# Kernel optimization log

Measured on AMD Instinct MI355X. Metric: run time of the kernel, lower is better.

## Reference

```python
import jax, jax.numpy as jnp
import numpy as np

N = 50000      # nodes
E = 800000     # edges (avg degree 16)
D_IN = 128
HID = 128
OUT = 64


def setup_inputs() -> dict:
    key = jax.random.key(0)
    ks = jax.random.split(key, 10)
    s = 0.05
    return {
        "node_feats": jax.random.normal(ks[0], (N, D_IN), jnp.float32),
        "edge_index": jax.random.randint(ks[1], (2, E), 0, N, jnp.int32),
        "W1": jax.random.normal(ks[2], (D_IN, HID), jnp.float32) * s,
        "b1": jnp.zeros((HID,), jnp.float32),
        "W2": jax.random.normal(ks[3], (HID, HID), jnp.float32) * s,
        "b2": jnp.zeros((HID,), jnp.float32),
        "W3": jax.random.normal(ks[4], (HID, OUT), jnp.float32) * s,
        "b3": jnp.zeros((OUT,), jnp.float32),
        "skip_W": jax.random.normal(ks[5], (HID, OUT), jnp.float32) * s,
        "skip_b": jnp.zeros((OUT,), jnp.float32),
    }


def _gcn(h, src, dst, out_norm, in_norm, W, b):
    # DGL GraphConv, norm='both': scale src by out_deg^-1/2, sum over incoming
    # edges at dst, scale by in_deg^-1/2, then linear transform + bias.
    h = h * out_norm[:, None]                                   # [N, d]
    agg = jax.ops.segment_sum(h[src], dst, num_segments=N)      # [N, d]
    return (agg * in_norm[:, None]) @ W + b


def reference(node_feats, edge_index, W1, b1, W2, b2, W3, b3, skip_W, skip_b):
    src, dst = edge_index[0], edge_index[1]
    ones = jnp.ones((E,), jnp.float32)
    out_deg = jax.ops.segment_sum(ones, src, num_segments=N)
    in_deg = jax.ops.segment_sum(ones, dst, num_segments=N)
    out_norm = jnp.maximum(out_deg, 1.0) ** -0.5
    in_norm = jnp.maximum(in_deg, 1.0) ** -0.5

    # layer 0 (no skip) + ReLU
    h = jax.nn.relu(_gcn(node_feats, src, dst, out_norm, in_norm, W1, b1))
    # layer 1: same-dim residual blend + ReLU
    g2 = _gcn(h, src, dst, out_norm, in_norm, W2, b2)
    h = jax.nn.relu(0.6 * h + 0.4 * g2)
    # layer 2 (last, no ReLU): dims differ -> projected skip blend
    g3 = _gcn(h, src, dst, out_norm, in_norm, W3, b3)
    h = 0.6 * (h @ skip_W + skip_b) + 0.4 * g3
    return h[None]  # [1, N, OUT]
```

## Files before the change

kernel.cpp:

```cpp
#include <hip/hip_runtime.h>
#include <math.h>

#define TPB 256
#define CAP 64

__global__ __launch_bounds__(TPB) void k_count(const int* __restrict__ ei, int E,
                                               int* __restrict__ cnt, int* __restrict__ od,
                                               unsigned short* __restrict__ slots) {
    int t = blockIdx.x * TPB + threadIdx.x;
    int base = t * 4;
    if (base + 3 < E) {
        int4 s4 = *(const int4*)(ei + base);
        int4 d4 = *(const int4*)(ei + E + base);
        int p0 = atomicAdd(&cnt[d4.x], 1);
        int p1 = atomicAdd(&cnt[d4.y], 1);
        int p2 = atomicAdd(&cnt[d4.z], 1);
        int p3 = atomicAdd(&cnt[d4.w], 1);
        atomicAdd(&od[s4.x], 1);
        atomicAdd(&od[s4.y], 1);
        atomicAdd(&od[s4.z], 1);
        atomicAdd(&od[s4.w], 1);
        if (p0 < CAP) slots[(d4.x << 6) + p0] = (unsigned short)s4.x;
        if (p1 < CAP) slots[(d4.y << 6) + p1] = (unsigned short)s4.y;
        if (p2 < CAP) slots[(d4.z << 6) + p2] = (unsigned short)s4.z;
        if (p3 < CAP) slots[(d4.w << 6) + p3] = (unsigned short)s4.w;
    } else {
        for (int e = base; e < E; ++e) {
            int s = ei[e], d = ei[E + e];
            int pos = atomicAdd(&cnt[d], 1);
            if (pos < CAP) slots[(d << 6) + pos] = (unsigned short)s;
            atomicAdd(&od[s], 1);
        }
    }
}

__global__ __launch_bounds__(TPB) void k_norm(const int* __restrict__ od, const int* __restrict__ cnt,
                                              float* __restrict__ onr, float* __restrict__ rsq,
                                              float* __restrict__ inr, int N) {
    int i = blockIdx.x * TPB + threadIdx.x;
    if (i < N) {
        float o = fmaxf((float)od[i], 1.0f);
        float q = sqrtf(o);
        onr[i] = 1.0f / q;
        rsq[i] = q;
        inr[i] = 1.0f / sqrtf(fmaxf((float)cnt[i], 1.0f));
    }
}

template <bool WONR>
__global__ __launch_bounds__(TPB) void k_spmm(const float* __restrict__ h,
                                              const int* __restrict__ cnt,
                                              const unsigned short* __restrict__ slots,
                                              const float* __restrict__ onr, const float* __restrict__ inr,
                                              float* __restrict__ agg, int N) {
    int lane = threadIdx.x & 63;
    int r = blockIdx.x * 4 + (threadIdx.x >> 6);
    if (r >= N) return;
    int n = cnt[r]; if (n > CAP) n = CAP;
    const unsigned short* sl = slots + (r << 6);
    const float2* hp = (const float2*)h;
    float ax0 = 0.f, ay0 = 0.f, ax1 = 0.f, ay1 = 0.f;
    float ax2 = 0.f, ay2 = 0.f, ax3 = 0.f, ay3 = 0.f;
    int e = 0;
    for (; e + 7 < n; e += 8) {
        ushort4 qa = *(const ushort4*)(sl + e);
        ushort4 qb = *(const ushort4*)(sl + e + 4);
        float2 v0 = hp[qa.x * 64 + lane];
        float2 v1 = hp[qa.y * 64 + lane];
        float2 v2 = hp[qa.z * 64 + lane];
        float2 v3 = hp[qa.w * 64 + lane];
        float2 v4 = hp[qb.x * 64 + lane];
        float2 v5 = hp[qb.y * 64 + lane];
        float2 v6 = hp[qb.z * 64 + lane];
        float2 v7 = hp[qb.w * 64 + lane];
        if (WONR) {
            float w0 = onr[qa.x], w1 = onr[qa.y], w2 = onr[qa.z], w3 = onr[qa.w];
            float w4 = onr[qb.x], w5 = onr[qb.y], w6 = onr[qb.z], w7 = onr[qb.w];
            ax0 += w0 * v0.x + w1 * v1.x;  ay0 += w0 * v0.y + w1 * v1.y;
            ax1 += w2 * v2.x + w3 * v3.x;  ay1 += w2 * v2.y + w3 * v3.y;
            ax2 += w4 * v4.x + w5 * v5.x;  ay2 += w4 * v4.y + w5 * v5.y;
            ax3 += w6 * v6.x + w7 * v7.x;  ay3 += w6 * v6.y + w7 * v7.y;
        } else {
            ax0 += v0.x + v1.x;  ay0 += v0.y + v1.y;
            ax1 += v2.x + v3.x;  ay1 += v2.y + v3.y;
            ax2 += v4.x + v5.x;  ay2 += v4.y + v5.y;
            ax3 += v6.x + v7.x;  ay3 += v6.y + v7.y;
        }
    }
    for (; e + 3 < n; e += 4) {
        ushort4 qa = *(const ushort4*)(sl + e);
        float2 v0 = hp[qa.x * 64 + lane];
        float2 v1 = hp[qa.y * 64 + lane];
        float2 v2 = hp[qa.z * 64 + lane];
        float2 v3 = hp[qa.w * 64 + lane];
        if (WONR) {
            float w0 = onr[qa.x], w1 = onr[qa.y], w2 = onr[qa.z], w3 = onr[qa.w];
            ax0 += w0 * v0.x + w1 * v1.x;  ay0 += w0 * v0.y + w1 * v1.y;
            ax1 += w2 * v2.x + w3 * v3.x;  ay1 += w2 * v2.y + w3 * v3.y;
        } else {
            ax0 += v0.x + v1.x;  ay0 += v0.y + v1.y;
            ax1 += v2.x + v3.x;  ay1 += v2.y + v3.y;
        }
    }
    for (; e < n; ++e) {
        int s0 = sl[e];
        float2 v0 = hp[s0 * 64 + lane];
        float w0 = WONR ? onr[s0] : 1.0f;
        ax0 += w0 * v0.x;  ay0 += w0 * v0.y;
    }
    float sc = inr[r];
    float2 o;
    o.x = sc * ((ax0 + ax1) + (ax2 + ax3));
    o.y = sc * ((ay0 + ay1) + (ay2 + ay3));
    ((float2*)agg)[r * 64 + lane] = o;
}

__global__ __launch_bounds__(TPB) void k_spmm_final(const float* __restrict__ P,
                                                    const int* __restrict__ cnt,
                                                    const unsigned short* __restrict__ slots,
                                                    const float* __restrict__ inr,
                                                    const float* __restrict__ b3, const float* __restrict__ bs,
                                                    float* __restrict__ out, int N) {
    int lane = threadIdx.x & 63;
    int r = blockIdx.x * 4 + (threadIdx.x >> 6);
    if (r >= N) return;
    int n = cnt[r]; if (n > CAP) n = CAP;
    const unsigned short* sl = slots + (r << 6);
    const float* t = P + 64;
    float a0 = 0.f, a1 = 0.f, a2 = 0.f, a3 = 0.f;
    float a4 = 0.f, a5 = 0.f, a6 = 0.f, a7 = 0.f;
    int e = 0;
    for (; e + 7 < n; e += 8) {
        ushort4 qa = *(const ushort4*)(sl + e);
        ushort4 qb = *(const ushort4*)(sl + e + 4);
        a0 += t[qa.x * 128 + lane];
        a1 += t[qa.y * 128 + lane];
        a2 += t[qa.z * 128 + lane];
        a3 += t[qa.w * 128 + lane];
        a4 += t[qb.x * 128 + lane];
        a5 += t[qb.y * 128 + lane];
        a6 += t[qb.z * 128 + lane];
        a7 += t[qb.w * 128 + lane];
    }
    for (; e + 3 < n; e += 4) {
        ushort4 qa = *(const ushort4*)(sl + e);
        a0 += t[qa.x * 128 + lane];
        a1 += t[qa.y * 128 + lane];
        a2 += t[qa.z * 128 + lane];
        a3 += t[qa.w * 128 + lane];
    }
    for (; e < n; ++e) a0 += t[sl[e] * 128 + lane];
    float g3 = inr[r] * (((a0 + a1) + (a2 + a3)) + ((a4 + a5) + (a6 + a7))) + b3[lane];
    float skip = P[r * 128 + lane] + bs[lane];
    out[r * 64 + lane] = 0.6f * skip + 0.4f * g3;
}

template <int MODE>
__global__ __launch_bounds__(TPB) void k_gemm(const float* __restrict__ A,
                                              const float* __restrict__ Wa, const float* __restrict__ Wb,
                                              const float* __restrict__ bias, const float* __restrict__ H,
                                              const float* __restrict__ onr, const float* __restrict__ rsq,
                                              float* __restrict__ C, int N) {
    __shared__ float As[64][132];
    int t = threadIdx.x;
    int bm = blockIdx.x * 64;
#pragma unroll
    for (int rep = 0; rep < 8; ++rep) {
        int idx = rep * TPB + t;
        int i = idx >> 5;
        int k4 = (idx & 31) * 4;
        int row = bm + i;
        float4 v = make_float4(0.f, 0.f, 0.f, 0.f);
        if (row < N) {
            v = *(const float4*)(&A[row * 128 + k4]);
            if (MODE == 2) {
                float rs = rsq[row];
                v.x *= rs; v.y *= rs; v.z *= rs; v.w *= rs;
            }
        }
        *(float4*)(&As[i][k4]) = v;
    }
    __syncthreads();
    int tx = t & 31, ty = t >> 5;
    int j0 = tx * 4;
    const float* Wp;
    int jj, ldw;
    if (MODE == 2) { Wp = (j0 < 64) ? Wa : Wb; jj = j0 & 63; ldw = 64; }
    else           { Wp = Wa;                   jj = j0;      ldw = 128; }
    float4 acc[8];
#pragma unroll
    for (int q = 0; q < 8; ++q) acc[q] = make_float4(0.f, 0.f, 0.f, 0.f);
    for (int k = 0; k < 128; k += 4) {
        float4 w0 = *(const float4*)(&Wp[(k + 0) * ldw + jj]);
        float4 w1 = *(const float4*)(&Wp[(k + 1) * ldw + jj]);
        float4 w2 = *(const float4*)(&Wp[(k + 2) * ldw + jj]);
        float4 w3 = *(const float4*)(&Wp[(k + 3) * ldw + jj]);
#pragma unroll
        for (int q = 0; q < 8; ++q) {
            float4 a = *(const float4*)(&As[ty + 8 * q][k]);
            acc[q].x += a.x * w0.x + a.y * w1.x + a.z * w2.x + a.w * w3.x;
            acc[q].y += a.x * w0.y + a.y * w1.y + a.z * w2.y + a.w * w3.y;
            acc[q].z += a.x * w0.z + a.y * w1.z + a.z * w2.z + a.w * w3.z;
            acc[q].w += a.x * w0.w + a.y * w1.w + a.z * w2.w + a.w * w3.w;
        }
    }
    float4 bv = make_float4(0.f, 0.f, 0.f, 0.f);
    if (MODE != 2) bv = *(const float4*)(&bias[j0]);
#pragma unroll
    for (int q = 0; q < 8; ++q) {
        int row = bm + ty + 8 * q;
        if (row >= N) continue;
        float4 o;
        o.x = acc[q].x + bv.x;
        o.y = acc[q].y + bv.y;
        o.z = acc[q].z + bv.z;
        o.w = acc[q].w + bv.w;
        if (MODE == 1) {
            float hs = rsq[row];
            float4 h = *(const float4*)(&H[row * 128 + j0]);
            o.x = 0.6f * h.x * hs + 0.4f * o.x;
            o.y = 0.6f * h.y * hs + 0.4f * o.y;
            o.z = 0.6f * h.z * hs + 0.4f * o.z;
            o.w = 0.6f * h.w * hs + 0.4f * o.w;
        }
        if (MODE != 2) {
            float on = onr[row];
            o.x = fmaxf(o.x, 0.f) * on;
            o.y = fmaxf(o.y, 0.f) * on;
            o.z = fmaxf(o.z, 0.f) * on;
            o.w = fmaxf(o.w, 0.f) * on;
        } else if (j0 >= 64) {
            float on = onr[row];
            o.x *= on; o.y *= on; o.z *= on; o.w *= on;
        }
        *(float4*)(&C[row * 128 + j0]) = o;
    }
}

extern "C" void kernel_launch(void* const* d_in, const int* in_sizes, int n_in,
                              void* d_out, int out_size, void* d_ws, size_t ws_size,
                              hipStream_t stream) {
    const float* x  = (const float*)d_in[0];
    const int*   ei = (const int*)d_in[1];
    const float* W1 = (const float*)d_in[2];
    const float* b1 = (const float*)d_in[3];
    const float* W2 = (const float*)d_in[4];
    const float* b2 = (const float*)d_in[5];
    const float* W3 = (const float*)d_in[6];
    const float* b3 = (const float*)d_in[7];
    const float* Ws = (const float*)d_in[8];
    const float* bs = (const float*)d_in[9];
    float* out = (float*)d_out;

    int N = in_sizes[0] / 128;
    int E = in_sizes[1] / 2;

    char* p = (char*)d_ws;
    auto alloc = [&](size_t bytes) -> char* {
        char* r = p;
        p += (bytes + 255) & ~(size_t)255;
        return r;
    };
    size_t npad = ((size_t)N * 4 + 255) & ~(size_t)255;
    int*   cnt  = (int*)alloc(npad);
    int*   od   = (int*)alloc(npad);
    float* onr  = (float*)alloc((size_t)N * 4);
    float* rsq  = (float*)alloc((size_t)N * 4);
    float* inr  = (float*)alloc((size_t)N * 4);
    unsigned short* slots = (unsigned short*)alloc((size_t)N * CAP * 2);
    float* agg  = (float*)alloc((size_t)N * 128 * 4);
    float* h1s  = (float*)alloc((size_t)N * 128 * 4);
    float* h2s  = (float*)alloc((size_t)N * 128 * 4);
    (void)ws_size; (void)n_in; (void)out_size;

    int cBlocks = ((E + 3) / 4 + TPB - 1) / TPB;
    int nBlocks = (N + TPB - 1) / TPB;
    int spmmBlocks = (N + 3) / 4;
    int gemmBlocks = (N + 63) / 64;

    hipMemsetAsync(cnt, 0, npad * 2, stream);

    k_count<<<cBlocks, TPB, 0, stream>>>(ei, E, cnt, od, slots);
    k_norm<<<nBlocks, TPB, 0, stream>>>(od, cnt, onr, rsq, inr, N);

    k_spmm<true><<<spmmBlocks, TPB, 0, stream>>>(x, cnt, slots, onr, inr, agg, N);
    k_gemm<0><<<gemmBlocks, TPB, 0, stream>>>(agg, W1, nullptr, b1, nullptr, onr, rsq, h1s, N);
    k_spmm<false><<<spmmBlocks, TPB, 0, stream>>>(h1s, cnt, slots, nullptr, inr, agg, N);
    k_gemm<1><<<gemmBlocks, TPB, 0, stream>>>(agg, W2, nullptr, b2, h1s, onr, rsq, h2s, N);
    float* P = agg;
    k_gemm<2><<<gemmBlocks, TPB, 0, stream>>>(h2s, Ws, W3, nullptr, nullptr, onr, rsq, P, N);
    k_spmm_final<<<spmmBlocks, TPB, 0, stream>>>(P, cnt, slots, inr, b3, bs, out, N);
}
```

Before: 413.9 us.

## Gather fp16 copies of features in all three SpMM passes

Adds a pre-pass that scales the input features by the out-degree norm and stores them as fp16. The first two GEMMs' gather inputs and the projected layer-3 features are also emitted as fp16, so every SpMM gathers half-width rows and accumulates in fp32. The aim is to halve the random-gather bandwidth that dominates the SpMM kernels. The cost is an extra conversion kernel, extra fp16 stores from the GEMMs, and reduced precision on the aggregated inputs.

```diff
diff --git a/kernel.cpp b/kernel.cpp
--- a/kernel.cpp
+++ b/kernel.cpp
@@ -1,4 +1,5 @@
 #include <hip/hip_runtime.h>
+#include <hip/hip_fp16.h>
 #include <math.h>
 
 #define TPB 256
@@ -47,66 +48,66 @@
     }
 }
 
-template <bool WONR>
-__global__ __launch_bounds__(TPB) void k_spmm(const float* __restrict__ h,
-                                              const int* __restrict__ cnt,
-                                              const unsigned short* __restrict__ slots,
-                                              const float* __restrict__ onr, const float* __restrict__ inr,
-                                              float* __restrict__ agg, int N) {
+__global__ __launch_bounds__(TPB) void k_cvt(const float* __restrict__ x, const float* __restrict__ onr,
+                                             __half2* __restrict__ xh, int nF4) {
+    int i4 = blockIdx.x * TPB + threadIdx.x;
+    if (i4 >= nF4) return;
+    int row = i4 >> 5;
+    float on = onr[row];
+    float4 v = ((const float4*)x)[i4];
+    __half2 a = __floats2half2_rn(v.x * on, v.y * on);
+    __half2 b = __floats2half2_rn(v.z * on, v.w * on);
+    uint2 u;
+    u.x = *reinterpret_cast<unsigned int*>(&a);
+    u.y = *reinterpret_cast<unsigned int*>(&b);
+    ((uint2*)xh)[i4] = u;
+}
+
+__global__ __launch_bounds__(TPB) void k_spmmh(const __half2* __restrict__ hp,
+                                               const int* __restrict__ cnt,
+                                               const unsigned short* __restrict__ slots,
+                                               const float* __restrict__ inr,
+                                               float* __restrict__ agg, int N) {
     int lane = threadIdx.x & 63;
     int r = blockIdx.x * 4 + (threadIdx.x >> 6);
     if (r >= N) return;
     int n = cnt[r]; if (n > CAP) n = CAP;
     const unsigned short* sl = slots + (r << 6);
-    const float2* hp = (const float2*)h;
     float ax0 = 0.f, ay0 = 0.f, ax1 = 0.f, ay1 = 0.f;
     float ax2 = 0.f, ay2 = 0.f, ax3 = 0.f, ay3 = 0.f;
     int e = 0;
     for (; e + 7 < n; e += 8) {
         ushort4 qa = *(const ushort4*)(sl + e);
         ushort4 qb = *(const ushort4*)(sl + e + 4);
-        float2 v0 = hp[qa.x * 64 + lane];
-        float2 v1 = hp[qa.y * 64 + lane];
-        float2 v2 = hp[qa.z * 64 + lane];
-        float2 v3 = hp[qa.w * 64 + lane];
-        float2 v4 = hp[qb.x * 64 + lane];
-        float2 v5 = hp[qb.y * 64 + lane];
-        float2 v6 = hp[qb.z * 64 + lane];
-        float2 v7 = hp[qb.w * 64 + lane];
-        if (WONR) {
-            float w0 = onr[qa.x], w1 = onr[qa.y], w2 = onr[qa.z], w3 = onr[qa.w];
-            float w4 = onr[qb.x], w5 = onr[qb.y], w6 = onr[qb.z], w7 = onr[qb.w];
-            ax0 += w0 * v0.x + w1 * v1.x;  ay0 += w0 * v0.y + w1 * v1.y;
-            ax1 += w2 * v2.x + w3 * v3.x;  ay1 += w2 * v2.y + w3 * v3.y;
-            ax2 += w4 * v4.x + w5 * v5.x;  ay2 += w4 * v4.y + w5 * v5.y;
-            ax3 += w6 * v6.x + w7 * v7.x;  ay3 += w6 * v6.y + w7 * v7.y;
-        } else {
-            ax0 += v0.x + v1.x;  ay0 += v0.y + v1.y;
-            ax1 += v2.x + v3.x;  ay1 += v2.y + v3.y;
-            ax2 += v4.x + v5.x;  ay2 += v4.y + v5.y;
-            ax3 += v6.x + v7.x;  ay3 += v6.y + v7.y;
-        }
+        __half2 v0 = hp[qa.x * 64 + lane];
+        __half2 v1 = hp[qa.y * 64 + lane];
+        __half2 v2 = hp[qa.z * 64 + lane];
+        __half2 v3 = hp[qa.w * 64 + lane];
+        __half2 v4 = hp[qb.x * 64 + lane];
+        __half2 v5 = hp[qb.y * 64 + lane];
+        __half2 v6 = hp[qb.z * 64 + lane];
+        __half2 v7 = hp[qb.w * 64 + lane];
+        float2 f0 = __half22float2(v0), f1 = __half22float2(v1);
+        float2 f2 = __half22float2(v2), f3 = __half22float2(v3);
+        float2 f4 = __half22float2(v4), f5 = __half22float2(v5);
+        float2 f6 = __half22float2(v6), f7 = __half22float2(v7);
+        ax0 += f0.x + f1.x;  ay0 += f0.y + f1.y;
+        ax1 += f2.x + f3.x;  ay1 += f2.y + f3.y;
+        ax2 += f4.x + f5.x;  ay2 += f4.y + f5.y;
+        ax3 += f6.x + f7.x;  ay3 += f6.y + f7.y;
     }
     for (; e + 3 < n; e += 4) {
         ushort4 qa = *(const ushort4*)(sl + e);
-        float2 v0 = hp[qa.x * 64 + lane];
-        float2 v1 = hp[qa.y * 64 + lane];
-        float2 v2 = hp[qa.z * 64 + lane];
-        float2 v3 = hp[qa.w * 64 + lane];
-        if (WONR) {
-            float w0 = onr[qa.x], w1 = onr[qa.y], w2 = onr[qa.z], w3 = onr[qa.w];
-            ax0 += w0 * v0.x + w1 * v1.x;  ay0 += w0 * v0.y + w1 * v1.y;
-            ax1 += w2 * v2.x + w3 * v3.x;  ay1 += w2 * v2.y + w3 * v3.y;
-        } else {
-            ax0 += v0.x + v1.x;  ay0 += v0.y + v1.y;
-            ax1 += v2.x + v3.x;  ay1 += v2.y + v3.y;
-        }
+        float2 f0 = __half22float2(hp[qa.x * 64 + lane]);
+        float2 f1 = __half22float2(hp[qa.y * 64 + lane]);
+        float2 f2 = __half22float2(hp[qa.z * 64 + lane]);
+        float2 f3 = __half22float2(hp[qa.w * 64 + lane]);
+        ax0 += f0.x + f1.x;  ay0 += f0.y + f1.y;
+        ax1 += f2.x + f3.x;  ay1 += f2.y + f3.y;
     }
     for (; e < n; ++e) {
-        int s0 = sl[e];
-        float2 v0 = hp[s0 * 64 + lane];
-        float w0 = WONR ? onr[s0] : 1.0f;
-        ax0 += w0 * v0.x;  ay0 += w0 * v0.y;
+        float2 f0 = __half22float2(hp[sl[e] * 64 + lane]);
+        ax0 += f0.x;  ay0 += f0.y;
     }
     float sc = inr[r];
     float2 o;
@@ -115,7 +116,8 @@
     ((float2*)agg)[r * 64 + lane] = o;
 }
 
-__global__ __launch_bounds__(TPB) void k_spmm_final(const float* __restrict__ P,
+__global__ __launch_bounds__(TPB) void k_spmm_final(const float* __restrict__ Pskip,
+                                                    const __half* __restrict__ Ph,
                                                     const int* __restrict__ cnt,
                                                     const unsigned short* __restrict__ slots,
                                                     const float* __restrict__ inr,
@@ -126,32 +128,31 @@
     if (r >= N) return;
     int n = cnt[r]; if (n > CAP) n = CAP;
     const unsigned short* sl = slots + (r << 6);
-    const float* t = P + 64;
     float a0 = 0.f, a1 = 0.f, a2 = 0.f, a3 = 0.f;
     float a4 = 0.f, a5 = 0.f, a6 = 0.f, a7 = 0.f;
     int e = 0;
     for (; e + 7 < n; e += 8) {
         ushort4 qa = *(const ushort4*)(sl + e);
         ushort4 qb = *(const ushort4*)(sl + e + 4);
-        a0 += t[qa.x * 128 + lane];
-        a1 += t[qa.y * 128 + lane];
-        a2 += t[qa.z * 128 + lane];
-        a3 += t[qa.w * 128 + lane];
-        a4 += t[qb.x * 128 + lane];
-        a5 += t[qb.y * 128 + lane];
-        a6 += t[qb.z * 128 + lane];
-        a7 += t[qb.w * 128 + lane];
+        a0 += __half2float(Ph[qa.x * 64 + lane]);
+        a1 += __half2float(Ph[qa.y * 64 + lane]);
+        a2 += __half2float(Ph[qa.z * 64 + lane]);
+        a3 += __half2float(Ph[qa.w * 64 + lane]);
+        a4 += __half2float(Ph[qb.x * 64 + lane]);
+        a5 += __half2float(Ph[qb.y * 64 + lane]);
+        a6 += __half2float(Ph[qb.z * 64 + lane]);
+        a7 += __half2float(Ph[qb.w * 64 + lane]);
     }
     for (; e + 3 < n; e += 4) {
         ushort4 qa = *(const ushort4*)(sl + e);
-        a0 += t[qa.x * 128 + lane];
-        a1 += t[qa.y * 128 + lane];
-        a2 += t[qa.z * 128 + lane];
-        a3 += t[qa.w * 128 + lane];
-    }
-    for (; e < n; ++e) a0 += t[sl[e] * 128 + lane];
+        a0 += __half2float(Ph[qa.x * 64 + lane]);
+        a1 += __half2float(Ph[qa.y * 64 + lane]);
+        a2 += __half2float(Ph[qa.z * 64 + lane]);
+        a3 += __half2float(Ph[qa.w * 64 + lane]);
+    }
+    for (; e < n; ++e) a0 += __half2float(Ph[sl[e] * 64 + lane]);
     float g3 = inr[r] * (((a0 + a1) + (a2 + a3)) + ((a4 + a5) + (a6 + a7))) + b3[lane];
-    float skip = P[r * 128 + lane] + bs[lane];
+    float skip = Pskip[r * 64 + lane] + bs[lane];
     out[r * 64 + lane] = 0.6f * skip + 0.4f * g3;
 }
 
@@ -160,7 +161,7 @@
                                               const float* __restrict__ Wa, const float* __restrict__ Wb,
                                               const float* __restrict__ bias, const float* __restrict__ H,
                                               const float* __restrict__ onr, const float* __restrict__ rsq,
-                                              float* __restrict__ C, int N) {
+                                              float* __restrict__ C, __half* __restrict__ Ch, int N) {
     __shared__ float As[64][132];
     int t = threadIdx.x;
     int bm = blockIdx.x * 64;
@@ -229,11 +230,28 @@
             o.y = fmaxf(o.y, 0.f) * on;
             o.z = fmaxf(o.z, 0.f) * on;
             o.w = fmaxf(o.w, 0.f) * on;
-        } else if (j0 >= 64) {
-            float on = onr[row];
-            o.x *= on; o.y *= on; o.z *= on; o.w *= on;
-        }
-        *(float4*)(&C[row * 128 + j0]) = o;
+            *(float4*)(&C[row * 128 + j0]) = o;
+            if (MODE == 0) {
+                __half2 ha = __floats2half2_rn(o.x, o.y);
+                __half2 hb = __floats2half2_rn(o.z, o.w);
+                uint2 u;
+                u.x = *reinterpret_cast<unsigned int*>(&ha);
+                u.y = *reinterpret_cast<unsigned int*>(&hb);
+                *(uint2*)(&Ch[row * 128 + j0]) = u;
+            }
+        } else {
+            if (j0 < 64) {
+                *(float4*)(&C[row * 64 + j0]) = o;
+            } else {
+                float on = onr[row];
+                __half2 ha = __floats2half2_rn(o.x * on, o.y * on);
+                __half2 hb = __floats2half2_rn(o.z * on, o.w * on);
+                uint2 u;
+                u.x = *reinterpret_cast<unsigned int*>(&ha);
+                u.y = *reinterpret_cast<unsigned int*>(&hb);
+                *(uint2*)(&Ch[row * 64 + (j0 - 64)]) = u;
+            }
+        }
     }
 }
 
@@ -268,13 +286,19 @@
     float* rsq  = (float*)alloc((size_t)N * 4);
     float* inr  = (float*)alloc((size_t)N * 4);
     unsigned short* slots = (unsigned short*)alloc((size_t)N * CAP * 2);
+    __half* xh  = (__half*)alloc((size_t)N * 128 * 2);
     float* agg  = (float*)alloc((size_t)N * 128 * 4);
     float* h1s  = (float*)alloc((size_t)N * 128 * 4);
     float* h2s  = (float*)alloc((size_t)N * 128 * 4);
     (void)ws_size; (void)n_in; (void)out_size;
 
+    __half* h1h   = xh;
+    float*  Pskip = agg;
+    __half* Ph    = (__half*)(agg + (size_t)N * 64);
+
     int cBlocks = ((E + 3) / 4 + TPB - 1) / TPB;
     int nBlocks = (N + TPB - 1) / TPB;
+    int cvtBlocks = (N * 32 + TPB - 1) / TPB;
     int spmmBlocks = (N + 3) / 4;
     int gemmBlocks = (N + 63) / 64;
 
@@ -282,12 +306,12 @@
 
     k_count<<<cBlocks, TPB, 0, stream>>>(ei, E, cnt, od, slots);
     k_norm<<<nBlocks, TPB, 0, stream>>>(od, cnt, onr, rsq, inr, N);
-
-    k_spmm<true><<<spmmBlocks, TPB, 0, stream>>>(x, cnt, slots, onr, inr, agg, N);
-    k_gemm<0><<<gemmBlocks, TPB, 0, stream>>>(agg, W1, nullptr, b1, nullptr, onr, rsq, h1s, N);
-    k_spmm<false><<<spmmBlocks, TPB, 0, stream>>>(h1s, cnt, slots, nullptr, inr, agg, N);
-    k_gemm<1><<<gemmBlocks, TPB, 0, stream>>>(agg, W2, nullptr, b2, h1s, onr, rsq, h2s, N);
-    float* P = agg;
-    k_gemm<2><<<gemmBlocks, TPB, 0, stream>>>(h2s, Ws, W3, nullptr, nullptr, onr, rsq, P, N);
-    k_spmm_final<<<spmmBlocks, TPB, 0, stream>>>(P, cnt, slots, inr, b3, bs, out, N);
-}
+    k_cvt<<<cvtBlocks, TPB, 0, stream>>>(x, onr, (__half2*)xh, N * 32);
+
+    k_spmmh<<<spmmBlocks, TPB, 0, stream>>>((const __half2*)xh, cnt, slots, inr, agg, N);
+    k_gemm<0><<<gemmBlocks, TPB, 0, stream>>>(agg, W1, nullptr, b1, nullptr, onr, rsq, h1s, h1h, N);
+    k_spmmh<<<spmmBlocks, TPB, 0, stream>>>((const __half2*)h1h, cnt, slots, inr, agg, N);
+    k_gemm<1><<<gemmBlocks, TPB, 0, stream>>>(agg, W2, nullptr, b2, h1s, onr, rsq, h2s, nullptr, N);
+    k_gemm<2><<<gemmBlocks, TPB, 0, stream>>>(h2s, Ws, W3, nullptr, nullptr, onr, rsq, Pskip, Ph, N);
+    k_spmm_final<<<spmmBlocks, TPB, 0, stream>>>(Pskip, Ph, cnt, slots, inr, b3, bs, out, N);
+}
```

Result: faster. 376.4 us (-9.1%).
